# Optimization experiments

Measured on AMD Instinct MI355X. Metric: run time of the kernel, lower is better.

The kernel has to match this reference:

```python
import jax, jax.numpy as jnp
import numpy as np

B, T, D, H = 4, 2048, 1024, 16
DK = D // H
LN_EPS = 1e-5


def setup_inputs() -> dict:
    key = jax.random.key(0)
    ks = jax.random.split(key, 12)
    s = 1.0 / np.sqrt(D)
    inp = {
        'x': jax.random.normal(ks[0], (B, T, D), jnp.float32),
        'Wq': jax.random.normal(ks[1], (D, D), jnp.float32) * s,
        'bq': jnp.zeros((D,), jnp.float32),
        'Wk': jax.random.normal(ks[2], (D, D), jnp.float32) * s,
        'bk': jnp.zeros((D,), jnp.float32),
        'Wv': jax.random.normal(ks[3], (D, D), jnp.float32) * s,
        'bv': jnp.zeros((D,), jnp.float32),
        'Wo': jax.random.normal(ks[4], (D, D), jnp.float32) * s,
        'bo': jnp.zeros((D,), jnp.float32),
        'ln_g': jnp.ones((D,), jnp.float32),
        'ln_b': jnp.zeros((D,), jnp.float32),
    }
    return inp


def reference(x, Wq, bq, Wk, bk, Wv, bv, Wo, bo, ln_g, ln_b):
    b, t, d = x.shape
    scale = jnp.sqrt(jnp.asarray(DK, x.dtype))
    # QKV projections -> [b, h, t, dk]
    q = (x @ Wq + bq).reshape(b, t, H, DK).transpose(0, 2, 1, 3)
    k = (x @ Wk + bk).reshape(b, t, H, DK).transpose(0, 2, 1, 3)
    v = (x @ Wv + bv).reshape(b, t, H, DK).transpose(0, 2, 1, 3)
    scores = jnp.einsum('bhqd,bhkd->bhqk', q, k) / scale  # [b,h,t,t]
    mask = jnp.tril(jnp.ones((t, t), x.dtype))[None, None]  # [1,1,t,t]
    neg = jnp.finfo(x.dtype).min
    scores = jnp.where(mask == 0, neg, scores)
    attn = jax.nn.softmax(scores, axis=-1)
    # mask-renormalize (as in the torch module)
    attn = attn * mask
    denom = attn.sum(-1, keepdims=True)
    attn = jnp.where(denom > 0, attn / denom, jnp.zeros_like(attn))
    ctx = jnp.einsum('bhqk,bhkd->bhqd', attn, v)  # [b,h,t,dk]
    ctx = ctx.transpose(0, 2, 1, 3).reshape(b, t, d)
    out = ctx @ Wo + bo
    y = out + x  # residual
    mu = y.mean(-1, keepdims=True)
    var = ((y - mu) ** 2).mean(-1, keepdims=True)
    return (y - mu) / jnp.sqrt(var + LN_EPS) * ln_g + ln_b
```

## Files before the change

### kernel.cpp

```cpp
#include <hip/hip_runtime.h>


using u16 = unsigned short;
using u32 = unsigned int;
typedef _Float16 f16x8 __attribute__((ext_vector_type(8)));
typedef float f32x4 __attribute__((ext_vector_type(4)));
typedef unsigned short u16x8 __attribute__((ext_vector_type(8)));

template <bool B> struct BoolTag { static constexpr bool v = B; };

__device__ inline u16 f2h_bits(float f) {
    _Float16 h = (_Float16)f;
    return __builtin_bit_cast(u16, h);
}

__device__ __forceinline__ void gload16(const void* g, void* l) {
    __builtin_amdgcn_global_load_lds(
        (const __attribute__((address_space(1))) void*)g,
        (__attribute__((address_space(3))) void*)l, 16, 0, 0);
}

__global__ __launch_bounds__(256) void convert_x_kernel(const float* __restrict__ x,
                                                        u16* __restrict__ xb) {
    size_t i = ((size_t)blockIdx.x * 256 + threadIdx.x) * 8;
    float4 a = *(const float4*)(x + i);
    float4 b = *(const float4*)(x + i + 4);
    u16x8 o;
    o[0] = f2h_bits(a.x); o[1] = f2h_bits(a.y); o[2] = f2h_bits(a.z); o[3] = f2h_bits(a.w);
    o[4] = f2h_bits(b.x); o[5] = f2h_bits(b.y); o[6] = f2h_bits(b.z); o[7] = f2h_bits(b.w);
    *(u16x8*)(xb + i) = o;
}

__global__ __launch_bounds__(256) void convert_wt_kernel(const float* __restrict__ W,
                                                         u16* __restrict__ Wt) {
    __shared__ float ts[64][68];
    const int k0 = blockIdx.x * 64, n0 = blockIdx.y * 64;
    const int tid = threadIdx.x, rr = tid >> 3, c = tid & 7;
#pragma unroll
    for (int p = 0; p < 2; p++) {
        int k = p * 32 + rr;
        float4 u = *(const float4*)(W + (size_t)(k0 + k) * 1024 + n0 + c * 8);
        float4 w = *(const float4*)(W + (size_t)(k0 + k) * 1024 + n0 + c * 8 + 4);
        *(float4*)&ts[k][c * 8] = u;
        *(float4*)&ts[k][c * 8 + 4] = w;
    }
    __syncthreads();
#pragma unroll
    for (int p = 0; p < 2; p++) {
        int n = p * 32 + rr;
        u16 o[8];
#pragma unroll
        for (int j = 0; j < 8; j++) o[j] = f2h_bits(ts[c * 8 + j][n]);
        *(u16x8*)(Wt + (size_t)(n0 + n) * 1024 + k0 + c * 8) = *(u16x8*)o;
    }
}

__global__ __launch_bounds__(512) void gemm_qkv_kernel(
    const u16* __restrict__ A, const u16* __restrict__ Wt,
    const float* __restrict__ bq, const float* __restrict__ bk,
    const float* __restrict__ bv, u16* __restrict__ qo, u16* __restrict__ ko,
    u16* __restrict__ vo) {
    __shared__ u16 As[2][256 * 64];
    __shared__ u16 Bs[2][256 * 64];

    const int bid = blockIdx.x;
    const int wg = (bid & 7) * 48 + (bid >> 3);
    const int bx = wg / 12, by = wg % 12;
    const size_t row0 = (size_t)bx * 256;
    const size_t col0 = (size_t)by * 256;
    const int tid = threadIdx.x, lane = tid & 63;
    const int wid = tid >> 6, wm = wid >> 2, wn = wid & 3;
    const int l15 = lane & 15, lg = lane >> 4;
    const int rr = tid >> 3, c8 = tid & 7;
    const int scw = (c8 ^ (rr & 7)) * 8;

    f32x4 acc[8][4] = {};

    auto stage = [&](int kt, int p) {
        const int k0 = kt * 64;
#pragma unroll
        for (int h = 0; h < 2; h++)
#pragma unroll
            for (int j = 0; j < 2; j++) {
                const int rbase = h * 128 + j * 64;
                gload16(A + (row0 + rbase + rr) * 1024 + k0 + scw,
                        As[p] + rbase * 64 + tid * 8);
                gload16(Wt + (col0 + rbase + rr) * 1024 + k0 + scw,
                        Bs[p] + rbase * 64 + tid * 8);
            }
    };

    stage(0, 0);
    int p = 0;
    for (int kt = 0; kt < 16; kt++) {
        stage((kt + 1) & 15, p ^ 1);
        asm volatile("s_waitcnt vmcnt(8)" ::: "memory");
        __builtin_amdgcn_sched_barrier(0);
        __builtin_amdgcn_s_barrier();
        __builtin_amdgcn_sched_barrier(0);
        const u16* Ab = As[p];
        const u16* Bb = Bs[p];
#pragma unroll
        for (int kc = 0; kc < 2; kc++) {
            f16x8 bf[4], af[8];
#pragma unroll
            for (int n = 0; n < 4; n++) {
                int rb = wn * 64 + n * 16 + l15;
                bf[n] = *(const f16x8*)(Bb + rb * 64 + ((kc * 4 + lg) ^ (rb & 7)) * 8);
            }
#pragma unroll
            for (int m = 0; m < 8; m++) {
                int ra = wm * 128 + m * 16 + l15;
                af[m] = *(const f16x8*)(Ab + ra * 64 + ((kc * 4 + lg) ^ (ra & 7)) * 8);
            }
            __builtin_amdgcn_s_setprio(1);
#pragma unroll
            for (int m = 0; m < 8; m++)
#pragma unroll
                for (int n = 0; n < 4; n++)
                    acc[m][n] = __builtin_amdgcn_mfma_f32_16x16x32_f16(
                        af[m], bf[n], acc[m][n], 0, 0, 0);
            __builtin_amdgcn_s_setprio(0);
        }
        __builtin_amdgcn_sched_barrier(0);
        __builtin_amdgcn_s_barrier();
        p ^= 1;
    }

    const int zsel = by >> 2;
    u16* ob = zsel == 0 ? qo : (zsel == 1 ? ko : vo);
    const float* bias = zsel == 0 ? bq : (zsel == 1 ? bk : bv);
    const float qs = zsel == 0 ? 0.18033688f : 1.0f;
#pragma unroll
    for (int m = 0; m < 8; m++) {
#pragma unroll
        for (int n = 0; n < 4; n++) {
            size_t col = col0 + wn * 64 + n * 16 + l15;
            size_t colz = col & 1023;
            float bb = bias[colz];
#pragma unroll
            for (int r = 0; r < 4; r++) {
                size_t row = row0 + wm * 128 + m * 16 + lg * 4 + r;
                ob[row * 1024 + colz] = f2h_bits((acc[m][n][r] + bb) * qs);
            }
        }
    }
}

__global__ __launch_bounds__(256) void gemm_wo_kernel(
    const u16* __restrict__ A, const u16* __restrict__ W,
    const float* __restrict__ bias, float* __restrict__ outf,
    const float* __restrict__ xres) {
    constexpr int Kd = 1024, Nd = 1024;
    __shared__ u16 As[128 * 64];
    __shared__ u16 Bs[128 * 64];

    const int tid = threadIdx.x;
    const int lane = tid & 63;
    const int wid = tid >> 6;
    const int wr = wid >> 1, wc = wid & 1;
    const int l15 = lane & 15, lg = lane >> 4;
    const size_t row0 = (size_t)blockIdx.x * 128;
    const size_t col0 = (size_t)blockIdx.y * 128;

    const int rr = tid >> 3, c8 = tid & 7;
    const int scw = (c8 ^ (rr & 7)) * 8;

    f32x4 acc[4][4] = {};

    for (int k0 = 0; k0 < Kd; k0 += 64) {
#pragma unroll
        for (int j = 0; j < 4; j++) {
            gload16(A + (row0 + j * 32 + rr) * Kd + k0 + scw,
                    As + (j * 256 + wid * 64) * 8);
            gload16(W + (col0 + j * 32 + rr) * Kd + k0 + scw,
                    Bs + (j * 256 + wid * 64) * 8);
        }
        __syncthreads();
#pragma unroll
        for (int kk = 0; kk < 2; kk++) {
            f16x8 af[4], bf[4];
            const int kc = kk * 4 + lg;
#pragma unroll
            for (int m = 0; m < 4; m++) {
                int ra = wr * 64 + m * 16 + l15;
                af[m] = *(const f16x8*)(As + ra * 64 + (kc ^ (ra & 7)) * 8);
                int rb = wc * 64 + m * 16 + l15;
                bf[m] = *(const f16x8*)(Bs + rb * 64 + (kc ^ (rb & 7)) * 8);
            }
#pragma unroll
            for (int m = 0; m < 4; m++)
#pragma unroll
                for (int n = 0; n < 4; n++)
                    acc[m][n] = __builtin_amdgcn_mfma_f32_16x16x32_f16(
                        af[m], bf[n], acc[m][n], 0, 0, 0);
        }
        __syncthreads();
    }

#pragma unroll
    for (int m = 0; m < 4; m++) {
#pragma unroll
        for (int n = 0; n < 4; n++) {
            size_t col = col0 + wc * 64 + n * 16 + l15;
            float bb = bias[col];
#pragma unroll
            for (int r = 0; r < 4; r++) {
                size_t row = row0 + wr * 64 + m * 16 + lg * 4 + r;
                size_t idx = row * Nd + col;
                outf[idx] = acc[m][n][r] + bb + xres[idx];
            }
        }
    }
}

__global__ __launch_bounds__(256) void transpose_v_kernel(const u16* __restrict__ V,
                                                          u16* __restrict__ Vt) {
    __shared__ u16 ts[64][72];
    const int bh = blockIdx.y;
    const int b = bh >> 4, h = bh & 15;
    const int t0 = blockIdx.x * 64;
    const int tid = threadIdx.x, rr = tid >> 3, c = tid & 7;
#pragma unroll
    for (int p = 0; p < 2; p++) {
        int t = p * 32 + rr;
        *(u16x8*)&ts[t][c * 8] =
            *(const u16x8*)(V + ((size_t)b * 2048 + t0 + t) * 1024 + h * 64 + c * 8);
    }
    __syncthreads();
#pragma unroll
    for (int p = 0; p < 2; p++) {
        int d = p * 32 + rr;
        u16 o[8];
#pragma unroll
        for (int j = 0; j < 8; j++) o[j] = ts[c * 8 + j][d];
        *(u16x8*)(Vt + ((size_t)bh * 64 + d) * 2048 + t0 + c * 8) = *(u16x8*)o;
    }
}

__global__ __launch_bounds__(256) void attn_kernel(const u16* __restrict__ Q,
                                                   const u16* __restrict__ Kb,
                                                   const u16* __restrict__ Vt,
                                                   u16* __restrict__ ctx) {
    __shared__ u16 Ks[2][64 * 64];
    __shared__ u16 Vs[2][64 * 64];
    __shared__ u16 Ps[8][16 * 64];

    const int bh = blockIdx.x;
    const int b = bh >> 4, h = bh & 15;
    const int qb = 15 - (int)blockIdx.y;
    const int tid = threadIdx.x, lane = tid & 63, wid = tid >> 6;
    const int l15 = lane & 15, lg = lane >> 4;
    const int q0w = qb * 128 + wid * 32;
    const int send = qb * 128;

    const int rr = tid >> 3, c8 = tid & 7;
    const int scw = (c8 ^ (rr & 7)) * 8;
    const size_t kbase = ((size_t)b * 2048) * 1024 + h * 64 + scw;
    const size_t vbase = ((size_t)bh * 64 + rr) * 2048 + scw;

    f16x8 qv[2][2];
#pragma unroll
    for (int qf = 0; qf < 2; qf++) {
        size_t qoff = ((size_t)b * 2048 + q0w + qf * 16 + l15) * 1024 + h * 64 + lg * 8;
        qv[qf][0] = *(const f16x8*)(Q + qoff);
        qv[qf][1] = *(const f16x8*)(Q + qoff + 32);
    }

    const int swk0 = (lg ^ (l15 & 7)) * 8;
    const int swk1 = ((4 + lg) ^ (l15 & 7)) * 8;
    u16* Pw0 = Ps[wid * 2 + 0] + l15 * 64;
    u16* Pw1 = Ps[wid * 2 + 1] + l15 * 64;

    f32x4 acc[2][4] = {};
    float psum[2] = {0.0f, 0.0f};

    auto stage = [&](int s, int bf) {
#pragma unroll
        for (int ph = 0; ph < 2; ph++) {
            gload16(Kb + kbase + (size_t)(s + ph * 32 + rr) * 1024,
                    Ks[bf] + (ph * 256 + wid * 64) * 8);
            gload16(Vt + vbase + (size_t)(ph * 32) * 2048 + s,
                    Vs[bf] + (ph * 256 + wid * 64) * 8);
        }
    };

    auto body = [&](int s, int bf, auto maskc) {
        constexpr bool MASK = decltype(maskc)::v;
        f32x4 sc[2][4];
#pragma unroll
        for (int c = 0; c < 4; c++) {
            const u16* kp = Ks[bf] + (c * 16 + l15) * 64;
            f16x8 kf0 = *(const f16x8*)(kp + swk0);
            f16x8 kf1 = *(const f16x8*)(kp + swk1);
#pragma unroll
            for (int qf = 0; qf < 2; qf++) {
                f32x4 z = {};
                z = __builtin_amdgcn_mfma_f32_16x16x32_f16(kf0, qv[qf][0], z, 0, 0, 0);
                z = __builtin_amdgcn_mfma_f32_16x16x32_f16(kf1, qv[qf][1], z, 0, 0, 0);
                sc[qf][c] = z;
            }
        }
#pragma unroll
        for (int qf = 0; qf < 2; qf++) {
            u16* Pw = qf ? Pw1 : Pw0;
#pragma unroll
            for (int c = 0; c < 4; c++) {
                float pv[4];
#pragma unroll
                for (int r = 0; r < 4; r++) {
                    float e = __builtin_amdgcn_exp2f(fminf(sc[qf][c][r], 15.0f));
                    if (MASK) {
                        int kk = s + c * 16 + lg * 4 + r;
                        e = (kk <= q0w + qf * 16 + l15) ? e : 0.0f;
                    }
                    psum[qf] += e;
                    pv[r] = e;
                }
                uint2 w;
                w.x = __builtin_bit_cast(u32, __builtin_amdgcn_cvt_pkrtz(pv[0], pv[1]));
                w.y = __builtin_bit_cast(u32, __builtin_amdgcn_cvt_pkrtz(pv[2], pv[3]));
                int gsw = (((c * 2 + (lg >> 1)) ^ (l15 & 7)) << 3) + (lg & 1) * 4;
                *(uint2*)(Pw + gsw) = w;
            }
        }
        f16x8 pa0[2], pa1[2];
#pragma unroll
        for (int qf = 0; qf < 2; qf++) {
            const u16* Pw = qf ? Pw1 : Pw0;
            pa0[qf] = *(const f16x8*)(Pw + ((lg ^ (l15 & 7)) << 3));
            pa1[qf] = *(const f16x8*)(Pw + (((4 + lg) ^ (l15 & 7)) << 3));
        }
#pragma unroll
        for (int dt = 0; dt < 4; dt++) {
            const u16* vp = Vs[bf] + (dt * 16 + l15) * 64;
            f16x8 vf0 = *(const f16x8*)(vp + swk0);
            f16x8 vf1 = *(const f16x8*)(vp + swk1);
#pragma unroll
            for (int qf = 0; qf < 2; qf++) {
                acc[qf][dt] =
                    __builtin_amdgcn_mfma_f32_16x16x32_f16(pa0[qf], vf0, acc[qf][dt], 0, 0, 0);
                acc[qf][dt] =
                    __builtin_amdgcn_mfma_f32_16x16x32_f16(pa1[qf], vf1, acc[qf][dt], 0, 0, 0);
            }
        }
    };

    stage(0, 0);
    int cur = 0;
    for (int s = 0; s < send; s += 64) {
        __syncthreads();
        stage(s + 64, cur ^ 1);
        body(s, cur, BoolTag<false>{});
        cur ^= 1;
    }
    __syncthreads();
    stage(send + 64, cur ^ 1);
    body(send, cur, BoolTag<true>{});
    cur ^= 1;
    __syncthreads();
    if (wid >= 2) body(send + 64, cur, BoolTag<true>{});

#pragma unroll
    for (int qf = 0; qf < 2; qf++) {
        psum[qf] += __shfl_xor(psum[qf], 16);
        psum[qf] += __shfl_xor(psum[qf], 32);
    }
#pragma unroll
    for (int qf = 0; qf < 2; qf++) {
        float inv = 1.0f / psum[qf];
#pragma unroll
        for (int r = 0; r < 4; r++) {
            float ir = __shfl(inv, lg * 4 + r);
            size_t row = (size_t)b * 2048 + q0w + qf * 16 + lg * 4 + r;
#pragma unroll
            for (int dt = 0; dt < 4; dt++)
                ctx[row * 1024 + h * 64 + dt * 16 + l15] = f2h_bits(acc[qf][dt][r] * ir);
        }
    }
}

__global__ __launch_bounds__(256) void ln_kernel(const float* __restrict__ y,
                                                 const float* __restrict__ g,
                                                 const float* __restrict__ bb,
                                                 float* __restrict__ out) {
    const int r = blockIdx.x, tid = threadIdx.x;
    float4 v = *(const float4*)(y + (size_t)r * 1024 + tid * 4);
    float s = v.x + v.y + v.z + v.w;
    float sq = v.x * v.x + v.y * v.y + v.z * v.z + v.w * v.w;
#pragma unroll
    for (int ofs = 1; ofs < 64; ofs <<= 1) {
        s += __shfl_xor(s, ofs);
        sq += __shfl_xor(sq, ofs);
    }
    __shared__ float as[4], aq[4];
    if ((tid & 63) == 0) { as[tid >> 6] = s; aq[tid >> 6] = sq; }
    __syncthreads();
    s = as[0] + as[1] + as[2] + as[3];
    sq = aq[0] + aq[1] + aq[2] + aq[3];
    float mu = s * (1.0f / 1024.0f);
    float var = sq * (1.0f / 1024.0f) - mu * mu;
    float rstd = rsqrtf(var + 1e-5f);
    float4 gv = *(const float4*)(g + tid * 4);
    float4 bv = *(const float4*)(bb + tid * 4);
    float4 o4;
    o4.x = (v.x - mu) * rstd * gv.x + bv.x;
    o4.y = (v.y - mu) * rstd * gv.y + bv.y;
    o4.z = (v.z - mu) * rstd * gv.z + bv.z;
    o4.w = (v.w - mu) * rstd * gv.w + bv.w;
    *(float4*)(out + (size_t)r * 1024 + tid * 4) = o4;
}

extern "C" void kernel_launch(void* const* d_in, const int* in_sizes, int n_in,
                              void* d_out, int out_size, void* d_ws, size_t ws_size,
                              hipStream_t stream) {
    const float* x  = (const float*)d_in[0];
    const float* Wq = (const float*)d_in[1];
    const float* bq = (const float*)d_in[2];
    const float* Wk = (const float*)d_in[3];
    const float* bk = (const float*)d_in[4];
    const float* Wv = (const float*)d_in[5];
    const float* bv = (const float*)d_in[6];
    const float* Wo = (const float*)d_in[7];
    const float* bo = (const float*)d_in[8];
    const float* lg = (const float*)d_in[9];
    const float* lb = (const float*)d_in[10];
    float* out = (float*)d_out;

    char* ws = (char*)d_ws;
    u16* xb = (u16*)(ws + 0);
    u16* wt = (u16*)(ws + 16777216);
    u16* q  = (u16*)(ws + 25165824);
    u16* k  = (u16*)(ws + 41943040);
    u16* v  = (u16*)(ws + 58720256);
    u16* vt = (u16*)(ws + 75497472);
    u16* cx = (u16*)(ws + 92274688);
    float* y = (float*)(ws + 109051904);

    convert_x_kernel<<<4096, 256, 0, stream>>>(x, xb);
    dim3 gw(16, 16);
    convert_wt_kernel<<<gw, 256, 0, stream>>>(Wq, wt);
    convert_wt_kernel<<<gw, 256, 0, stream>>>(Wk, wt + 1048576);
    convert_wt_kernel<<<gw, 256, 0, stream>>>(Wv, wt + 2097152);
    convert_wt_kernel<<<gw, 256, 0, stream>>>(Wo, wt + 3145728);

    gemm_qkv_kernel<<<384, 512, 0, stream>>>(xb, wt, bq, bk, bv, q, k, v);
    transpose_v_kernel<<<dim3(32, 64), 256, 0, stream>>>(v, vt);
    attn_kernel<<<dim3(64, 16), 256, 0, stream>>>(q, k, vt, cx);
    gemm_wo_kernel<<<dim3(64, 8), 256, 0, stream>>>(cx, wt + 3145728, bo, y, x);
    ln_kernel<<<8192, 256, 0, stream>>>(y, lg, lb, out);
}
```

Measured before the change: 194.9 us.

## Unify QKV and output GEMMs into triple-buffered 128x256 tiled kernel

Both projection GEMMs now go through one templated kernel with 128x256 output tiles, 512 threads, and a three-stage LDS ring. Each stage's loads are split into two halves issued inside the k-chunk loop, so global-to-LDS traffic overlaps the MFMAs, with fine-grained vmcnt waits and barriers per chunk. The QKV GEMM gets smaller tiles and twice as many blocks, which should improve occupancy and wave balance across CUs. The output GEMM moves from 128x128 with 4 waves and no prefetch to the pipelined 256-wide tile. The cost is more barriers per iteration and more LDS per block (three stages).

After: 202.5 us. +3.9%, slower.

```diff
diff --git a/kernel.cpp b/kernel.cpp
--- a/kernel.cpp
+++ b/kernel.cpp
@@ -55,160 +55,127 @@
     }
 }
 
-__global__ __launch_bounds__(512) void gemm_qkv_kernel(
+template <int MODE>
+__global__ __launch_bounds__(512) void gemm256_kernel(
     const u16* __restrict__ A, const u16* __restrict__ Wt,
-    const float* __restrict__ bq, const float* __restrict__ bk,
-    const float* __restrict__ bv, u16* __restrict__ qo, u16* __restrict__ ko,
-    u16* __restrict__ vo) {
-    __shared__ u16 As[2][256 * 64];
-    __shared__ u16 Bs[2][256 * 64];
+    const float* __restrict__ b0, const float* __restrict__ b1,
+    const float* __restrict__ b2, u16* __restrict__ qo, u16* __restrict__ ko,
+    u16* __restrict__ vo, float* __restrict__ outf,
+    const float* __restrict__ xres) {
+    constexpr int NBY = (MODE == 0) ? 12 : 4;
+    __shared__ u16 As[3][128 * 64];
+    __shared__ u16 Bs[3][256 * 64];
 
     const int bid = blockIdx.x;
-    const int wg = (bid & 7) * 48 + (bid >> 3);
-    const int bx = wg / 12, by = wg % 12;
-    const size_t row0 = (size_t)bx * 256;
+    const int cpx = (MODE == 0) ? 96 : 32;
+    const int swz = (bid & 7) * cpx + (bid >> 3);
+    const int bx = swz / NBY, by = swz % NBY;
+    const size_t row0 = (size_t)bx * 128;
     const size_t col0 = (size_t)by * 256;
+
     const int tid = threadIdx.x, lane = tid & 63;
     const int wid = tid >> 6, wm = wid >> 2, wn = wid & 3;
     const int l15 = lane & 15, lg = lane >> 4;
     const int rr = tid >> 3, c8 = tid & 7;
     const int scw = (c8 ^ (rr & 7)) * 8;
 
-    f32x4 acc[8][4] = {};
-
-    auto stage = [&](int kt, int p) {
+    f32x4 acc[4][4] = {};
+
+    auto stage_half = [&](int kt, int p, int h) {
         const int k0 = kt * 64;
-#pragma unroll
-        for (int h = 0; h < 2; h++)
-#pragma unroll
-            for (int j = 0; j < 2; j++) {
-                const int rbase = h * 128 + j * 64;
-                gload16(A + (row0 + rbase + rr) * 1024 + k0 + scw,
-                        As[p] + rbase * 64 + tid * 8);
-                gload16(Wt + (col0 + rbase + rr) * 1024 + k0 + scw,
-                        Bs[p] + rbase * 64 + tid * 8);
-            }
+        if (h == 0) {
+            gload16(A + (row0 + rr) * 1024 + k0 + scw, As[p] + tid * 8);
+            gload16(Wt + (col0 + rr) * 1024 + k0 + scw, Bs[p] + tid * 8);
+            gload16(Wt + (col0 + 64 + rr) * 1024 + k0 + scw,
+                    Bs[p] + (512 + tid) * 8);
+        } else {
+            gload16(A + (row0 + 64 + rr) * 1024 + k0 + scw,
+                    As[p] + (512 + tid) * 8);
+            gload16(Wt + (col0 + 128 + rr) * 1024 + k0 + scw,
+                    Bs[p] + (1024 + tid) * 8);
+            gload16(Wt + (col0 + 192 + rr) * 1024 + k0 + scw,
+                    Bs[p] + (1536 + tid) * 8);
+        }
     };
 
-    stage(0, 0);
-    int p = 0;
-    for (int kt = 0; kt < 16; kt++) {
-        stage((kt + 1) & 15, p ^ 1);
-        asm volatile("s_waitcnt vmcnt(8)" ::: "memory");
-        __builtin_amdgcn_sched_barrier(0);
-        __builtin_amdgcn_s_barrier();
-        __builtin_amdgcn_sched_barrier(0);
+    stage_half(0, 0, 0); stage_half(0, 0, 1);
+    stage_half(1, 1, 0); stage_half(1, 1, 1);
+    asm volatile("s_waitcnt vmcnt(6)" ::: "memory");
+    __builtin_amdgcn_s_barrier();
+
+    int p = 0, pn = 1, pp = 2;
+    for (int t = 0; t < 16; t++) {
+        const bool st = (t + 2 < 16);
         const u16* Ab = As[p];
         const u16* Bb = Bs[p];
 #pragma unroll
         for (int kc = 0; kc < 2; kc++) {
-            f16x8 bf[4], af[8];
+            if (st) stage_half(t + 2, pp, kc);
+            f16x8 af[4], bf[4];
 #pragma unroll
             for (int n = 0; n < 4; n++) {
                 int rb = wn * 64 + n * 16 + l15;
                 bf[n] = *(const f16x8*)(Bb + rb * 64 + ((kc * 4 + lg) ^ (rb & 7)) * 8);
             }
 #pragma unroll
-            for (int m = 0; m < 8; m++) {
-                int ra = wm * 128 + m * 16 + l15;
+            for (int m = 0; m < 4; m++) {
+                int ra = wm * 64 + m * 16 + l15;
                 af[m] = *(const f16x8*)(Ab + ra * 64 + ((kc * 4 + lg) ^ (ra & 7)) * 8);
             }
+            __builtin_amdgcn_sched_barrier(0);
+            if (kc == 1) {
+                if (st) asm volatile("s_waitcnt vmcnt(6)" ::: "memory");
+                else    asm volatile("s_waitcnt vmcnt(0)" ::: "memory");
+                __builtin_amdgcn_sched_barrier(0);
+            }
+            __builtin_amdgcn_s_barrier();
+            __builtin_amdgcn_sched_barrier(0);
             __builtin_amdgcn_s_setprio(1);
 #pragma unroll
-            for (int m = 0; m < 8; m++)
+            for (int m = 0; m < 4; m++)
 #pragma unroll
                 for (int n = 0; n < 4; n++)
                     acc[m][n] = __builtin_amdgcn_mfma_f32_16x16x32_f16(
                         af[m], bf[n], acc[m][n], 0, 0, 0);
             __builtin_amdgcn_s_setprio(0);
-        }
-        __builtin_amdgcn_sched_barrier(0);
-        __builtin_amdgcn_s_barrier();
-        p ^= 1;
-    }
-
-    const int zsel = by >> 2;
-    u16* ob = zsel == 0 ? qo : (zsel == 1 ? ko : vo);
-    const float* bias = zsel == 0 ? bq : (zsel == 1 ? bk : bv);
-    const float qs = zsel == 0 ? 0.18033688f : 1.0f;
-#pragma unroll
-    for (int m = 0; m < 8; m++) {
-#pragma unroll
-        for (int n = 0; n < 4; n++) {
-            size_t col = col0 + wn * 64 + n * 16 + l15;
-            size_t colz = col & 1023;
-            float bb = bias[colz];
-#pragma unroll
-            for (int r = 0; r < 4; r++) {
-                size_t row = row0 + wm * 128 + m * 16 + lg * 4 + r;
-                ob[row * 1024 + colz] = f2h_bits((acc[m][n][r] + bb) * qs);
-            }
-        }
-    }
-}
-
-__global__ __launch_bounds__(256) void gemm_wo_kernel(
-    const u16* __restrict__ A, const u16* __restrict__ W,
-    const float* __restrict__ bias, float* __restrict__ outf,
-    const float* __restrict__ xres) {
-    constexpr int Kd = 1024, Nd = 1024;
-    __shared__ u16 As[128 * 64];
-    __shared__ u16 Bs[128 * 64];
-
-    const int tid = threadIdx.x;
-    const int lane = tid & 63;
-    const int wid = tid >> 6;
-    const int wr = wid >> 1, wc = wid & 1;
-    const int l15 = lane & 15, lg = lane >> 4;
-    const size_t row0 = (size_t)blockIdx.x * 128;
-    const size_t col0 = (size_t)blockIdx.y * 128;
-
-    const int rr = tid >> 3, c8 = tid & 7;
-    const int scw = (c8 ^ (rr & 7)) * 8;
-
-    f32x4 acc[4][4] = {};
-
-    for (int k0 = 0; k0 < Kd; k0 += 64) {
-#pragma unroll
-        for (int j = 0; j < 4; j++) {
-            gload16(A + (row0 + j * 32 + rr) * Kd + k0 + scw,
-                    As + (j * 256 + wid * 64) * 8);
-            gload16(W + (col0 + j * 32 + rr) * Kd + k0 + scw,
-                    Bs + (j * 256 + wid * 64) * 8);
-        }
-        __syncthreads();
-#pragma unroll
-        for (int kk = 0; kk < 2; kk++) {
-            f16x8 af[4], bf[4];
-            const int kc = kk * 4 + lg;
-#pragma unroll
-            for (int m = 0; m < 4; m++) {
-                int ra = wr * 64 + m * 16 + l15;
-                af[m] = *(const f16x8*)(As + ra * 64 + (kc ^ (ra & 7)) * 8);
-                int rb = wc * 64 + m * 16 + l15;
-                bf[m] = *(const f16x8*)(Bs + rb * 64 + (kc ^ (rb & 7)) * 8);
-            }
-#pragma unroll
-            for (int m = 0; m < 4; m++)
-#pragma unroll
-                for (int n = 0; n < 4; n++)
-                    acc[m][n] = __builtin_amdgcn_mfma_f32_16x16x32_f16(
-                        af[m], bf[n], acc[m][n], 0, 0, 0);
-        }
-        __syncthreads();
-    }
-
-#pragma unroll
-    for (int m = 0; m < 4; m++) {
-#pragma unroll
-        for (int n = 0; n < 4; n++) {
-            size_t col = col0 + wc * 64 + n * 16 + l15;
-            float bb = bias[col];
-#pragma unroll
-            for (int r = 0; r < 4; r++) {
-                size_t row = row0 + wr * 64 + m * 16 + lg * 4 + r;
-                size_t idx = row * Nd + col;
-                outf[idx] = acc[m][n][r] + bb + xres[idx];
+            __builtin_amdgcn_sched_barrier(0);
+            __builtin_amdgcn_s_barrier();
+        }
+        int tmp = p; p = pn; pn = pp; pp = tmp;
+    }
+
+    if (MODE == 0) {
+        const int zsel = by >> 2;
+        u16* ob = zsel == 0 ? qo : (zsel == 1 ? ko : vo);
+        const float* bias = zsel == 0 ? b0 : (zsel == 1 ? b1 : b2);
+        const float qs = zsel == 0 ? 0.18033688f : 1.0f;
+#pragma unroll
+        for (int m = 0; m < 4; m++) {
+#pragma unroll
+            for (int n = 0; n < 4; n++) {
+                size_t col = col0 + wn * 64 + n * 16 + l15;
+                size_t colz = col & 1023;
+                float bb = bias[colz];
+#pragma unroll
+                for (int r = 0; r < 4; r++) {
+                    size_t row = row0 + wm * 64 + m * 16 + lg * 4 + r;
+                    ob[row * 1024 + colz] = f2h_bits((acc[m][n][r] + bb) * qs);
+                }
+            }
+        }
+    } else {
+#pragma unroll
+        for (int m = 0; m < 4; m++) {
+#pragma unroll
+            for (int n = 0; n < 4; n++) {
+                size_t col = col0 + wn * 64 + n * 16 + l15;
+                float bb = b0[col];
+#pragma unroll
+                for (int r = 0; r < 4; r++) {
+                    size_t row = row0 + wm * 64 + m * 16 + lg * 4 + r;
+                    size_t idx = row * 1024 + col;
+                    outf[idx] = acc[m][n][r] + bb + xres[idx];
+                }
             }
         }
     }
@@ -444,9 +411,12 @@
     convert_wt_kernel<<<gw, 256, 0, stream>>>(Wv, wt + 2097152);
     convert_wt_kernel<<<gw, 256, 0, stream>>>(Wo, wt + 3145728);
 
-    gemm_qkv_kernel<<<384, 512, 0, stream>>>(xb, wt, bq, bk, bv, q, k, v);
+    gemm256_kernel<0><<<768, 512, 0, stream>>>(xb, wt, bq, bk, bv, q, k, v,
+                                               nullptr, nullptr);
     transpose_v_kernel<<<dim3(32, 64), 256, 0, stream>>>(v, vt);
     attn_kernel<<<dim3(64, 16), 256, 0, stream>>>(q, k, vt, cx);
-    gemm_wo_kernel<<<dim3(64, 8), 256, 0, stream>>>(cx, wt + 3145728, bo, y, x);
+    gemm256_kernel<1><<<256, 512, 0, stream>>>(cx, wt + 3145728, bo, nullptr,
+                                               nullptr, nullptr, nullptr, nullptr,
+                                               y, x);
     ln_kernel<<<8192, 256, 0, stream>>>(y, lg, lb, out);
 }
```
